# Kernel tuning notes

Hardware: AMD Instinct MI355X
Metric: run time of the kernel (lower is better)

## Reference

```python
import jax, jax.numpy as jnp
import numpy as np
from jax import lax

PERM = (0, 1, 4, 5, 2, 3)  # swap the two (H,W) spatial pairs
DN = ('NCHWXY', 'OIHWXY', 'NCHWXY')  # 4 spatial dims -> native 4D conv


def conv4d(x, w, b):
    # x: [B,Ci,S,S,S,S], w: [Co,Ci,k1,k1,k2,k2], 'SAME' padding as in ANCNet Conv4d
    y = lax.conv_general_dilated(x, w, window_strides=(1, 1, 1, 1),
                                 padding='SAME', dimension_numbers=DN)
    return y + b[None, :, None, None, None, None]


def setup_inputs() -> dict:
    key = jax.random.key(0)
    ks = jax.random.split(key, 10)
    B, S = 2, 25
    def w_init(k, shape):
        fan_in = shape[1] * np.prod(shape[2:])
        return jax.random.normal(k, shape, jnp.float32) * (1.0 / np.sqrt(fan_in))
    return {
        'x': jax.random.normal(ks[0], (B, 1, S, S, S, S), jnp.float32),
        'w0': w_init(ks[1], (8, 1, 3, 3, 5, 5)),   'b0': jnp.zeros((8,), jnp.float32),
        'w1': w_init(ks[2], (8, 1, 5, 5, 5, 5)),   'b1': jnp.zeros((8,), jnp.float32),
        'w2a': w_init(ks[3], (16, 16, 5, 5, 5, 5)), 'b2a': jnp.zeros((16,), jnp.float32),
        'w2b': w_init(ks[4], (1, 16, 5, 5, 5, 5)),  'b2b': jnp.zeros((1,), jnp.float32),
    }


def reference(x, w0, b0, w1, b1, w2a, b2a, w2b, b2b):
    relu = jax.nn.relu
    conv0 = lambda t: relu(conv4d(t, w0, b0))
    conv1 = lambda t: relu(conv4d(t, w1, b1))
    conv2 = lambda t: relu(conv4d(relu(conv4d(t, w2a, b2a)), w2b, b2b))
    sym = lambda f, t: f(t) + jnp.transpose(f(jnp.transpose(t, PERM)), PERM)
    x0 = sym(conv0, x)
    x1 = sym(conv1, x)
    h = jnp.concatenate((x0, x1), axis=1)  # [B,16,S,S,S,S]
    return sym(conv2, h)
```

## Files before the change

### kernel.cpp

```cpp
#include <hip/hip_runtime.h>

#define S 25
#define PLANE 625
#define VOL 390625
#define CLn 12500000
#define HREG2 7168
#define LDSPAD 20224

typedef __attribute__((ext_vector_type(8))) short short8;
typedef __attribute__((ext_vector_type(4))) float f32x4;
typedef __attribute__((ext_vector_type(16))) float f32x16;
typedef __attribute__((ext_vector_type(4))) unsigned short us4;
typedef __attribute__((ext_vector_type(4))) unsigned int u32x4;

__device__ __forceinline__ unsigned short f2bf(float f) {
    unsigned int u = __float_as_uint(f);
    u += 0x7fffu + ((u >> 16) & 1u);
    return (unsigned short)(u >> 16);
}

__device__ __forceinline__ void glds16(const unsigned short* g, unsigned short* l) {
    __builtin_amdgcn_global_load_lds(
        (const __attribute__((address_space(1))) unsigned int*)g,
        (__attribute__((address_space(3))) unsigned int*)l, 16, 0, 0);
}

__device__ __forceinline__ int xcd_swz(int orig, int nwg) {
    int q = nwg >> 3, r = nwg & 7;
    int x = orig & 7, lid = orig >> 3;
    return (x < r ? x * (q + 1) : r * (q + 1) + (x - r) * q) + lid;
}

__device__ __forceinline__ int nxt_kd(int kd, int d0, int d1) {
    #pragma unroll 1
    for (++kd; kd < 25; ++kd) {
        int kd0 = kd / 5, kd1 = kd - kd0 * 5;
        int e0 = d0 + kd0 - 2, e1 = d1 + kd1 - 2;
        if (e0 >= 0 && e0 < S && e1 >= 0 && e1 < S) return kd;
    }
    return 25;
}

__device__ __forceinline__ int nxt_w(int uv, int U, int V, int b0, int b1) {
    #pragma unroll 1
    for (++uv; uv < U * V; ++uv) {
        int u = uv / V, v = uv - u * V;
        int e0 = b0 + u, e1 = b1 + v;
        if (e0 >= 0 && e0 < S && e1 >= 0 && e1 < S) return uv;
    }
    return U * V;
}

__global__ __launch_bounds__(256) void prep_weights(
    const float* __restrict__ w2a, const float* __restrict__ w2b,
    const float* __restrict__ w0, const float* __restrict__ w1,
    unsigned short* __restrict__ wbig32, unsigned short* __restrict__ wl1,
    unsigned short* __restrict__ wcp, unsigned short* __restrict__ z16)
{
    int idx = blockIdx.x * 256 + threadIdx.x;
    if (idx < 320000) {
        int k = idx & 15;
        int m = (idx >> 4) & 31;
        int rem = idx >> 9;
        int t = rem % 25, kd01 = rem / 25;
        float v;
        if (m < 16) v = w2a[(m * 16 + k) * 625 + kd01 * 25 + t];
        else        v = w2a[((m - 16) * 16 + k) * 625 + t * 25 + kd01];
        wbig32[idx] = f2bf(v);
    } else if (idx < 345600) {
        int j = idx - 320000;
        int k = j & 31;
        int row = (j >> 5) & 15;
        int tile = (j >> 9) & 1;
        int kd01 = j >> 10;
        int kd0 = kd01 / 5, kd1 = kd01 - kd0 * 5;
        float v = 0.f;
        if (k < 25) {
            int t = k, kd2 = t / 5, kd3 = t - kd2 * 5;
            if (tile == 0) {
                v = (row < 8) ? w1[row * 625 + kd0 * 125 + kd1 * 25 + t]
                              : w1[(row - 8) * 625 + t * 25 + kd01];
            } else {
                if (row < 8) {
                    if (kd0 >= 1 && kd0 <= 3 && kd1 >= 1 && kd1 <= 3)
                        v = w0[((row * 3 + (kd0 - 1)) * 3 + (kd1 - 1)) * 25 + t];
                } else {
                    if (kd2 >= 1 && kd2 <= 3 && kd3 >= 1 && kd3 <= 3)
                        v = w0[(row - 8) * 225 + ((kd2 - 1) * 3 + (kd3 - 1)) * 25 + kd01];
                }
            }
        }
        wl1[j] = f2bf(v);
    } else if (idx < 345600 + 614400) {
        int j = idx - 345600;
        int k = j & 31;
        int row = (j >> 5) & 15;
        int rem = j >> 9;
        int t = rem % 25, uv = rem / 25;
        int u = uv >> 3, v8 = uv & 7;
        int path = row & 1, o = row >> 1;
        int py = o >> 2, px = o & 3;
        int kd0 = u - py, kd1 = v8 - px;
        float v = 0.f;
        if (kd0 >= 0 && kd0 < 5 && kd1 >= 0 && kd1 < 5) {
            int ci = k & 15;
            if (path == 0 && k < 16)
                v = w2b[ci * 625 + (kd0 * 5 + kd1) * 25 + t];
            else if (path == 1 && k >= 16)
                v = w2b[ci * 625 + t * 25 + kd0 * 5 + kd1];
        }
        wcp[j] = f2bf(v);
    } else if (idx < 345600 + 614400 + 8) {
        z16[idx - 960000] = 0;
    }
}

__global__ __launch_bounds__(256) void layer1_mfma(
    const float* __restrict__ x, const unsigned short* __restrict__ wl1,
    const float* __restrict__ b0, const float* __restrict__ b1,
    unsigned short* __restrict__ hbf)
{
    __shared__ __align__(16) unsigned short pl[29 * 32];
    const int blk = blockIdx.x;
    const int b = blk / PLANE;
    const int d01 = blk - b * PLANE;
    const int d0 = d01 / S, d1 = d01 - d0 * S;
    const int tid = threadIdx.x;
    const int l = tid & 63, w = tid >> 6;
    const int col = l & 15, kq = l >> 4;

    int off[8];
    #pragma unroll
    for (int j = 0; j < 8; ++j) {
        int t = kq * 8 + j; if (t > 24) t = 24;
        int t5 = t / 5;
        off[j] = t5 * 32 + (t - t5 * 5);
    }
    int rb[10];
    #pragma unroll
    for (int g = 0; g < 10; ++g) {
        int n = (w * 10 + g) * 16 + col; if (n > 624) n = 624;
        int d2 = n / 25;
        rb[g] = d2 * 32 + (n - d2 * 25);
    }

    f32x4 acc0[10], acc1[10];
    #pragma unroll
    for (int g = 0; g < 10; ++g) {
        acc0[g] = (f32x4){0.f, 0.f, 0.f, 0.f};
        acc1[g] = (f32x4){0.f, 0.f, 0.f, 0.f};
    }

    const float* xb = x + (size_t)b * VOL;

    #pragma unroll 1
    for (int kd01 = 0; kd01 < 25; ++kd01) {
        const int kd0 = kd01 / 5, kd1 = kd01 - kd0 * 5;
        const int e0 = d0 + kd0 - 2, e1 = d1 + kd1 - 2;
        if (e0 < 0 || e0 >= S || e1 < 0 || e1 >= S) continue;
        __syncthreads();
        {
            const float* sp = xb + (e0 * 25 + e1) * 625;
            for (int i = tid; i < 841; i += 256) {
                int r = i / 29, c = i - r * 29;
                float v = 0.f;
                if (r >= 2 && r <= 26 && c >= 2 && c <= 26)
                    v = sp[(r - 2) * 25 + (c - 2)];
                pl[r * 32 + c] = f2bf(v);
            }
        }
        __syncthreads();
        const unsigned short* wp = wl1 + kd01 * 1024;
        short8 a0 = *(const short8*)(wp + col * 32 + kq * 8);
        short8 a1 = *(const short8*)(wp + 512 + col * 32 + kq * 8);
        #pragma unroll
        for (int g = 0; g < 10; ++g) {
            short8 bf;
            #pragma unroll
            for (int j = 0; j < 8; ++j)
                bf[j] = (short)pl[rb[g] + off[j]];
            acc0[g] = __builtin_amdgcn_mfma_f32_16x16x32_bf16(a0, bf, acc0[g], 0, 0, 0);
            acc1[g] = __builtin_amdgcn_mfma_f32_16x16x32_bf16(a1, bf, acc1[g], 0, 0, 0);
        }
    }

    const int ch = (kq & 1) * 4;
    float bi1[4], bi0[4];
    #pragma unroll
    for (int r = 0; r < 4; ++r) { bi1[r] = b1[ch + r]; bi0[r] = b0[ch + r]; }
    const bool lo = (kq < 2);
    const size_t obase = (size_t)(b * 625 + d01) * 625;
    #pragma unroll
    for (int g = 0; g < 10; ++g) {
        int n = (w * 10 + g) * 16 + col;
        float r0[4], r1[4];
        #pragma unroll
        for (int r = 0; r < 4; ++r) {
            r0[r] = fmaxf(acc0[g][r] + bi1[r], 0.f);
            r1[r] = fmaxf(acc1[g][r] + bi0[r], 0.f);
        }
        us4 u0, u1;
        #pragma unroll
        for (int r = 0; r < 4; ++r) {
            float p0 = __shfl_xor(r0[r], 32, 64);
            float p1 = __shfl_xor(r1[r], 32, 64);
            u0[r] = f2bf(r0[r] + p0);
            u1[r] = f2bf(r1[r] + p1);
        }
        if (lo && n < 625) {
            *(us4*)&hbf[(obase + n) * 16 + 8 + ch] = u0;
            *(us4*)&hbf[(obase + n) * 16 + ch]     = u1;
        }
    }
}

__global__ __launch_bounds__(256, 3) void conv_mfma32(
    const unsigned short* __restrict__ in, const unsigned short* __restrict__ wq,
    const float* __restrict__ bias, const unsigned short* __restrict__ z16,
    unsigned short* __restrict__ gA, unsigned short* __restrict__ gB)
{
    __shared__ __align__(16) unsigned short pl[LDSPAD];
    const int blk = xcd_swz(blockIdx.x, 1250);
    const int b = blk / PLANE;
    const int d01 = blk - b * PLANE;
    const int d0 = d01 / S, d1 = d01 - d0 * S;
    const int tid = threadIdx.x;
    const int l = tid & 63, w = tid >> 6;
    const int h = l >> 5;
    const int nl = l & 31;

    int srcofs[7]; bool okz[7];
    #pragma unroll
    for (int j = 0; j < 7; ++j) {
        int cid = (j * 4 + w) * 64 + l;
        int half = (cid >= 896) ? 1 : 0;
        int pt = cid - half * 896;
        int r = pt / 29, c = pt - r * 29;
        okz[j] = (pt < 841) && (r >= 2 && r <= 26 && c >= 2 && c <= 26);
        srcofs[j] = ((r - 2) * 25 + (c - 2)) * 16 + half * 8;
    }

    int rbo[5];
    #pragma unroll
    for (int g = 0; g < 5; ++g) {
        int n = (w * 5 + g) * 32 + nl;
        if (n > 624) n = 624;
        int d2 = n / 25, d3 = n - d2 * 25;
        rbo[g] = h * HREG2 + (d2 * 29 + d3) * 8;
    }

    f32x16 acc[5];
    #pragma unroll
    for (int g = 0; g < 5; ++g)
        #pragma unroll
        for (int r = 0; r < 16; ++r) acc[g][r] = 0.f;

    const unsigned short* inb = in + (size_t)b * 6250000;

    int kd_cur = nxt_kd(-1, d0, d1);
    {
        int kd0 = kd_cur / 5, kd1 = kd_cur - kd0 * 5;
        const unsigned short* sb = inb + (size_t)((d0 + kd0 - 2) * 25 + (d1 + kd1 - 2)) * 10000;
        #pragma unroll
        for (int j = 0; j < 7; ++j)
            glds16(okz[j] ? sb + srcofs[j] : z16, &pl[(j * 4 + w) * 512]);
    }

    #pragma unroll 1
    while (kd_cur < 25) {
        const int kd01 = kd_cur;
        const int kd_nxt = nxt_kd(kd_cur, d0, d1);
        __syncthreads();

        const unsigned short* wkd = wq + (size_t)kd01 * 12800 + nl * 16 + h * 8;
        #pragma unroll 1
        for (int t = 0; t < 25; ++t) {
            short8 a = *(const short8*)(wkd + t * 512);
            int t5 = t / 5;
            int toff = (t5 * 29 + (t - t5 * 5)) * 8;
            #pragma unroll
            for (int g = 0; g < 5; ++g) {
                short8 bf = *(const short8*)&pl[rbo[g] + toff];
                acc[g] = __builtin_amdgcn_mfma_f32_32x32x16_bf16(a, bf, acc[g], 0, 0, 0);
            }
        }

        __syncthreads();
        if (kd_nxt < 25) {
            int kd0 = kd_nxt / 5, kd1 = kd_nxt - kd0 * 5;
            const unsigned short* sb = inb + (size_t)((d0 + kd0 - 2) * 25 + (d1 + kd1 - 2)) * 10000;
            #pragma unroll
            for (int j = 0; j < 7; ++j)
                glds16(okz[j] ? sb + srcofs[j] : z16, &pl[(j * 4 + w) * 512]);
        }
        kd_cur = kd_nxt;
    }

    #pragma unroll
    for (int g = 0; g < 5; ++g) {
        int n = (w * 5 + g) * 32 + nl;
        if (n < 625) {
            size_t ob = ((size_t)(b * 625 + d01) * 625 + n) * 16;
            #pragma unroll
            for (int q = 0; q < 4; ++q) {
                int baserow = q * 8 + 4 * h;
                us4 u;
                #pragma unroll
                for (int r = 0; r < 4; ++r) {
                    int co = (baserow + r) & 15;
                    u[r] = f2bf(fmaxf(acc[g][q * 4 + r] + bias[co], 0.f));
                }
                if (baserow < 16) *(us4*)&gA[ob + baserow] = u;
                else              *(us4*)&gB[ob + baserow - 16] = u;
            }
        }
    }
}

__global__ __launch_bounds__(128, 2) void convc_v3(
    const unsigned short* __restrict__ gA,
    const unsigned short* __restrict__ wcp, const float* __restrict__ b2b,
    float* __restrict__ outp)
{
    __shared__ __align__(16) unsigned short pl[348 * 36];
    const int blk = xcd_swz(blockIdx.x, 728);
    const int q = blk & 3;
    const int geo = blk >> 2;
    const int b = geo / 91;
    const int g91 = geo - b * 91;
    const int t0 = g91 / 7, t1 = g91 - t0 * 7;
    const int D0 = t0 * 2, D1 = t1 * 4;
    const int r0 = (q == 0) ? -2 : (q == 1) ? 4 : (q == 2) ? 10 : 17;
    const int tid = threadIdx.x;
    const int l = tid & 63, w = tid >> 6;
    const int col = l & 15, kq = l >> 4;

    int ofsG[11], ofsL[11]; bool ok[11];
    #pragma unroll
    for (int j = 0; j < 11; ++j) {
        int cid = tid + j * 128;
        int p = cid >> 2, qq = cid & 3;
        int r = p / 29, c = p - r * 29;
        int d2e = r + r0, d3e = c - 2;
        ok[j] = (cid < 1392) && (d2e >= 0 && d2e < S) && (d3e >= 0 && d3e < S);
        ofsG[j] = (qq >> 1) * CLn + (d2e * 25 + d3e) * 16 + (qq & 1) * 8;
        ofsL[j] = p * 36 + qq * 8;
    }

    int rb[5];
    #pragma unroll
    for (int g = 0; g < 5; ++g) {
        int n = q * 160 + (w * 5 + g) * 16 + col; if (n > 624) n = 624;
        int d2 = n / 25;
        rb[g] = ((d2 - r0 - 2) * 29 + (n - d2 * 25)) * 36;
    }

    f32x4 acc[5];
    #pragma unroll
    for (int g = 0; g < 5; ++g) acc[g] = (f32x4){0.f, 0.f, 0.f, 0.f};

    const unsigned short* gAb = gA + (size_t)b * 6250000;

    u32x4 stg[11];
    int uv_cur = nxt_w(-1, 6, 8, D0 - 2, D1 - 2);
    {
        int u = uv_cur >> 3, v = uv_cur & 7;
        const unsigned short* sb = gAb + (size_t)((D0 - 2 + u) * 25 + (D1 - 2 + v)) * 10000;
        #pragma unroll
        for (int j = 0; j < 11; ++j) {
            u32x4 z = {0u, 0u, 0u, 0u};
            if (ok[j]) z = *(const u32x4*)(sb + ofsG[j]);
            stg[j] = z;
        }
    }

    #pragma unroll 1
    while (uv_cur < 48) {
        const int uvc = uv_cur;
        const int uv_nxt = nxt_w(uv_cur, 6, 8, D0 - 2, D1 - 2);
        __syncthreads();
        #pragma unroll
        for (int j = 0; j < 11; ++j)
            if (j < 10 || tid < 112) *(u32x4*)&pl[ofsL[j]] = stg[j];
        __syncthreads();
        if (uv_nxt < 48) {
            int u = uv_nxt >> 3, v = uv_nxt & 7;
            const unsigned short* sb = gAb + (size_t)((D0 - 2 + u) * 25 + (D1 - 2 + v)) * 10000;
            #pragma unroll
            for (int j = 0; j < 11; ++j) {
                u32x4 z = {0u, 0u, 0u, 0u};
                if (ok[j]) z = *(const u32x4*)(sb + ofsG[j]);
                stg[j] = z;
            }
        }

        const unsigned short* wbase = wcp + (size_t)uvc * 12800;
        #pragma unroll 1
        for (int t = 0; t < 25; ++t) {
            const int t5 = t / 5;
            const int toff = (t5 * 29 + (t - t5 * 5)) * 36;
            short8 a = *(const short8*)(wbase + (t * 16 + col) * 32 + kq * 8);
            #pragma unroll
            for (int g = 0; g < 5; ++g) {
                short8 bf = *(const short8*)&pl[rb[g] + toff + kq * 8];
                acc[g] = __builtin_amdgcn_mfma_f32_16x16x32_bf16(a, bf, acc[g], 0, 0, 0);
            }
        }
        uv_cur = uv_nxt;
    }

    const float bv = b2b[0];
    #pragma unroll
    for (int g = 0; g < 5; ++g) {
        int n = q * 160 + (w * 5 + g) * 16 + col;
        if (n < 625) {
            #pragma unroll
            for (int r2 = 0; r2 < 2; ++r2) {
                int o = kq * 2 + r2;
                int d0 = D0 + (o >> 2), d1 = D1 + (o & 3);
                if (d0 < S && d1 < S) {
                    float vA = acc[g][r2 * 2], vB = acc[g][r2 * 2 + 1];
                    outp[((size_t)b * 625 + d0 * 25 + d1) * 625 + n] =
                        fmaxf(vA + bv, 0.f) + fmaxf(vB + bv, 0.f);
                }
            }
        }
    }
}

extern "C" void kernel_launch(void* const* d_in, const int* in_sizes, int n_in,
                              void* d_out, int out_size, void* d_ws, size_t ws_size,
                              hipStream_t stream) {
    const float* x   = (const float*)d_in[0];
    const float* w0  = (const float*)d_in[1];
    const float* b0  = (const float*)d_in[2];
    const float* w1  = (const float*)d_in[3];
    const float* b1  = (const float*)d_in[4];
    const float* w2a = (const float*)d_in[5];
    const float* b2a = (const float*)d_in[6];
    const float* w2b = (const float*)d_in[7];
    const float* b2b = (const float*)d_in[8];
    float* out = (float*)d_out;

    unsigned short* hbf    = (unsigned short*)d_ws;
    unsigned short* gA     = hbf + CLn;
    unsigned short* gB     = gA + CLn;
    unsigned short* wbig32 = gB + CLn;
    unsigned short* wl1    = wbig32 + 320000;
    unsigned short* wcp    = wl1 + 25600;
    unsigned short* z16    = wcp + 614400;
    if (ws_size < ((size_t)3 * CLn + 320000 + 25600 + 614400 + 8) * sizeof(unsigned short)) return;

    prep_weights<<<3751, 256, 0, stream>>>(w2a, w2b, w0, w1, wbig32, wl1, wcp, z16);
    layer1_mfma<<<1250, 256, 0, stream>>>(x, wl1, b0, b1, hbf);
    conv_mfma32<<<1250, 256, 0, stream>>>(hbf, wbig32, b2a, z16, gA, gB);
    convc_v3<<<728, 128, 0, stream>>>(gA, wcp, b2b, out);
}
```

Before: 959.9 us.

## Split final conv reduction across two blocks and add finalize kernel

The last conv kernel now splits its spatial-weight loop over u into two halves, each handled by a separate block. This doubles the grid from 728 to 1456 blocks to improve occupancy and latency hiding. Partial sums go to a float workspace, and a new finalize kernel adds the halves, applies bias and ReLU, and sums the symmetric pair. The cost is an extra launch plus about 12.5 MB of extra global writes and reads for the partials.

```diff
diff --git a/kernel.cpp b/kernel.cpp
--- a/kernel.cpp
+++ b/kernel.cpp
@@ -41,14 +41,14 @@
     return 25;
 }
 
-__device__ __forceinline__ int nxt_w(int uv, int U, int V, int b0, int b1) {
+__device__ __forceinline__ int nxt_wr(int uv, int uhi, int b0, int b1) {
     #pragma unroll 1
-    for (++uv; uv < U * V; ++uv) {
-        int u = uv / V, v = uv - u * V;
+    for (++uv; uv < uhi * 8; ++uv) {
+        int u = uv >> 3, v = uv & 7;
         int e0 = b0 + u, e1 = b1 + v;
         if (e0 >= 0 && e0 < S && e1 >= 0 && e1 < S) return uv;
     }
-    return U * V;
+    return uhi * 8;
 }
 
 __global__ __launch_bounds__(256) void prep_weights(
@@ -319,17 +319,20 @@
 
 __global__ __launch_bounds__(128, 2) void convc_v3(
     const unsigned short* __restrict__ gA,
-    const unsigned short* __restrict__ wcp, const float* __restrict__ b2b,
-    float* __restrict__ outp)
+    const unsigned short* __restrict__ wcp,
+    float* __restrict__ part)
 {
     __shared__ __align__(16) unsigned short pl[348 * 36];
-    const int blk = xcd_swz(blockIdx.x, 728);
-    const int q = blk & 3;
-    const int geo = blk >> 2;
+    const int blk = xcd_swz(blockIdx.x, 1456);
+    const int hw = blk & 1;
+    const int rest = blk >> 1;
+    const int q = rest & 3;
+    const int geo = rest >> 2;
     const int b = geo / 91;
     const int g91 = geo - b * 91;
     const int t0 = g91 / 7, t1 = g91 - t0 * 7;
     const int D0 = t0 * 2, D1 = t1 * 4;
+    const int ulo = 3 * hw, uhi = 3 * hw + 3;
     const int r0 = (q == 0) ? -2 : (q == 1) ? 4 : (q == 2) ? 10 : 17;
     const int tid = threadIdx.x;
     const int l = tid & 63, w = tid >> 6;
@@ -362,8 +365,8 @@
     const unsigned short* gAb = gA + (size_t)b * 6250000;
 
     u32x4 stg[11];
-    int uv_cur = nxt_w(-1, 6, 8, D0 - 2, D1 - 2);
-    {
+    int uv_cur = nxt_wr(ulo * 8 - 1, uhi, D0 - 2, D1 - 2);
+    if (uv_cur < uhi * 8) {
         int u = uv_cur >> 3, v = uv_cur & 7;
         const unsigned short* sb = gAb + (size_t)((D0 - 2 + u) * 25 + (D1 - 2 + v)) * 10000;
         #pragma unroll
@@ -375,15 +378,15 @@
     }
 
     #pragma unroll 1
-    while (uv_cur < 48) {
+    while (uv_cur < uhi * 8) {
         const int uvc = uv_cur;
-        const int uv_nxt = nxt_w(uv_cur, 6, 8, D0 - 2, D1 - 2);
+        const int uv_nxt = nxt_wr(uv_cur, uhi, D0 - 2, D1 - 2);
         __syncthreads();
         #pragma unroll
         for (int j = 0; j < 11; ++j)
             if (j < 10 || tid < 112) *(u32x4*)&pl[ofsL[j]] = stg[j];
         __syncthreads();
-        if (uv_nxt < 48) {
+        if (uv_nxt < uhi * 8) {
             int u = uv_nxt >> 3, v = uv_nxt & 7;
             const unsigned short* sb = gAb + (size_t)((D0 - 2 + u) * 25 + (D1 - 2 + v)) * 10000;
             #pragma unroll
@@ -409,7 +412,6 @@
         uv_cur = uv_nxt;
     }
 
-    const float bv = b2b[0];
     #pragma unroll
     for (int g = 0; g < 5; ++g) {
         int n = q * 160 + (w * 5 + g) * 16 + col;
@@ -419,13 +421,27 @@
                 int o = kq * 2 + r2;
                 int d0 = D0 + (o >> 2), d1 = D1 + (o & 3);
                 if (d0 < S && d1 < S) {
-                    float vA = acc[g][r2 * 2], vB = acc[g][r2 * 2 + 1];
-                    outp[((size_t)b * 625 + d0 * 25 + d1) * 625 + n] =
-                        fmaxf(vA + bv, 0.f) + fmaxf(vB + bv, 0.f);
+                    size_t pidx = (size_t)(d0 * 25 + d1) * 625 + n;
+                    part[((size_t)((hw * 2 + 0) * 2 + b)) * VOL + pidx] = acc[g][r2 * 2];
+                    part[((size_t)((hw * 2 + 1) * 2 + b)) * VOL + pidx] = acc[g][r2 * 2 + 1];
                 }
             }
         }
     }
+}
+
+__global__ __launch_bounds__(256) void convc_fin(
+    const float* __restrict__ part, const float* __restrict__ b2b,
+    float* __restrict__ outp)
+{
+    int idx = blockIdx.x * 256 + threadIdx.x;
+    if (idx >= 2 * VOL) return;
+    int b = idx / VOL;
+    int p = idx - b * VOL;
+    const float bv = b2b[0];
+    float A = part[(size_t)(0 * 2 + b) * VOL + p] + part[(size_t)(4 + b) * VOL + p];
+    float B = part[(size_t)(2 + b) * VOL + p] + part[(size_t)(6 + b) * VOL + p];
+    outp[idx] = fmaxf(A + bv, 0.f) + fmaxf(B + bv, 0.f);
 }
 
 extern "C" void kernel_launch(void* const* d_in, const int* in_sizes, int n_in,
@@ -449,10 +465,13 @@
     unsigned short* wl1    = wbig32 + 320000;
     unsigned short* wcp    = wl1 + 25600;
     unsigned short* z16    = wcp + 614400;
-    if (ws_size < ((size_t)3 * CLn + 320000 + 25600 + 614400 + 8) * sizeof(unsigned short)) return;
+    float* part = (float*)(z16 + 8);
+    if (ws_size < ((size_t)3 * CLn + 320000 + 25600 + 614400 + 8) * sizeof(unsigned short)
+                  + (size_t)8 * VOL * sizeof(float)) return;
 
     prep_weights<<<3751, 256, 0, stream>>>(w2a, w2b, w0, w1, wbig32, wl1, wcp, z16);
     layer1_mfma<<<1250, 256, 0, stream>>>(x, wl1, b0, b1, hbf);
     conv_mfma32<<<1250, 256, 0, stream>>>(hbf, wbig32, b2a, z16, gA, gB);
-    convc_v3<<<728, 128, 0, stream>>>(gA, wcp, b2b, out);
-}
+    convc_v3<<<1456, 128, 0, stream>>>(gA, wcp, part);
+    convc_fin<<<3052, 256, 0, stream>>>(part, b2b, out);
+}
```

New measurement: 817.6 us, median of 2. 14.8% less time.
